# Optimization experiments

Measured on AMD Instinct MI355X. Metric: run time of the kernel, lower is better.

## Reference

```python
import jax, jax.numpy as jnp
import numpy as np

NUM_CLUSTERS = 64
NUM_ITERS = 3
TEMPERATURE = 0.1
CENTER_EMA = 0.99


def _l2norm(x, eps=1e-12):
    n = jnp.linalg.norm(x, axis=-1, keepdims=True)
    return x / jnp.maximum(n, eps)


def setup_inputs() -> dict:
    key = jax.random.key(0)
    k1, k2 = jax.random.split(key)
    B, N, d = 16, 4096, 768
    features = jax.random.normal(k1, (B, N, d), dtype=jnp.float32)
    centers = jax.random.normal(k2, (NUM_CLUSTERS, d), dtype=jnp.float32)
    return {"features": features, "centers": centers}


def reference(features, centers):
    B, N, d = features.shape
    K = centers.shape[0]
    M = B * N  # single-device: M_total == M_local

    features_norm = _l2norm(features)          # [B, N, d]
    centers_n = _l2norm(centers)               # [K, d]

    logits = jnp.einsum('bnd,kd->bnk', features_norm, centers_n) / TEMPERATURE
    Q = jnp.exp(logits.astype(jnp.float32).reshape(M, K).T)  # [K, M]

    Q = Q / jnp.maximum(Q.sum(), 1e-12)
    for _ in range(NUM_ITERS):
        row_sums = Q.sum(axis=1, keepdims=True)              # [K, 1]
        Q = Q / (jnp.maximum(row_sums, 1e-12) * float(K))
        col_sums = Q.sum(axis=0, keepdims=True)              # [1, M]
        Q = Q / (jnp.maximum(col_sums, 1e-12) * float(M))

    assignments = (Q * float(M)).T.reshape(B, N, K).astype(features.dtype)

    # EMA center update
    Q_flat = assignments.reshape(M, K)
    feat_flat = features_norm.reshape(M, d)
    weighted = jnp.einsum('mk,md->kd', Q_flat, feat_flat)    # [K, d]
    mass = Q_flat.sum(axis=0)                                # [K]
    new_centers = _l2norm(weighted / jnp.maximum(mass, 1e-6)[:, None])
    updated = CENTER_EMA * centers_n + (1.0 - CENTER_EMA) * new_centers
    updated = _l2norm(updated)

    return assignments, updated
```

## Files before the change

### kernel.cpp

```cpp
#include <hip/hip_runtime.h>
#include <hip/hip_bf16.h>

#define M_TOTAL 65536
#define DIM 768
#define KC 64
#define INV_T 10.0f

#define DT 128
#define MB 64
#define CH 8
#define MSEG 128

#define LOGITS_BLOCKS (M_TOTAL / 64)
#define SROWS 128
#define SINK_BLOCKS (M_TOTAL / SROWS)
#define PSG_ROWS 64

typedef __attribute__((ext_vector_type(4))) float f32x4;
typedef __attribute__((ext_vector_type(8))) short bf16x8;
typedef __attribute__((ext_vector_type(4))) unsigned short u16x4;

__device__ __forceinline__ short f2bf(float f) {
    __hip_bfloat16 h = __float2bfloat16(f);
    union { __hip_bfloat16 h; short s; } u; u.h = h;
    return u.s;
}

__global__ __launch_bounds__(256) void k_centers(const float* __restrict__ centers,
                                                 float* __restrict__ cn,
                                                 short* __restrict__ cnbf,
                                                 float* __restrict__ psg) {
    int k = blockIdx.x, tid = threadIdx.x;
    psg[k * 256 + tid] = 0.f;
    float ss = 0.f;
    for (int i = tid; i < DIM; i += 256) { float v = centers[k * DIM + i]; ss += v * v; }
    __shared__ float red[4];
    for (int o = 32; o; o >>= 1) ss += __shfl_xor(ss, o);
    if ((tid & 63) == 0) red[tid >> 6] = ss;
    __syncthreads();
    ss = red[0] + red[1] + red[2] + red[3];
    float inv = 1.0f / fmaxf(sqrtf(ss), 1e-12f);
    for (int i = tid; i < DIM; i += 256) {
        float v = centers[k * DIM + i] * inv;
        cn[k * DIM + i] = v;
        cnbf[k * DIM + i] = f2bf(v);
    }
}

__global__ __launch_bounds__(256) void k_logits(const float* __restrict__ F,
                                                const short* __restrict__ cnbf,
                                                float* __restrict__ E,
                                                float* __restrict__ invn,
                                                float* __restrict__ PSG0) {
    __shared__ float fbuf[3][4][1024];
    __shared__ float bsr[4][KC];
    int tid = threadIdx.x;
    int wave = tid >> 6, lane = tid & 63;
    int l15 = lane & 15, lhi = lane >> 4;
    int rowbase = blockIdx.x * 64;

    int srow_l = lane >> 4;
    int c4 = lane & 15;

#define STAGE(t_, b_)                                                                     \
    do {                                                                                  \
        _Pragma("unroll") for (int i_ = 0; i_ < 4; ++i_) {                                \
            int r_ = i_ * 4 + srow_l;                                \
            const float* src_ = F + (size_t)(rowbase + wave * 16 + r_) * DIM + (t_) * 64  \
                                + (((c4 ^ (r_ & 7)) << 2));                               \
            float* dst_ = &fbuf[b_][wave][i_ * 256];                                      \
            __builtin_amdgcn_global_load_lds(                                             \
                (const __attribute__((address_space(1))) void*)src_,                      \
                (__attribute__((address_space(3))) void*)dst_, 16, 0, 0);                 \
        }                                                                                 \
    } while (0)

    STAGE(0, 0);
    STAGE(1, 1);

    f32x4 acc[4];
#pragma unroll
    for (int n = 0; n < 4; ++n) acc[n] = (f32x4){0.f, 0.f, 0.f, 0.f};
    float ss = 0.f;

    const short* Bb = cnbf + (size_t)l15 * DIM + lhi * 8;
    int swz = (l15 & 7) << 2;

#pragma unroll
    for (int t = 0; t < 12; ++t) {
        bf16x8 b[8];
#pragma unroll
        for (int n = 0; n < 4; ++n) {
            b[n * 2]     = *(const bf16x8*)(Bb + (size_t)n * 16 * DIM + t * 64);
            b[n * 2 + 1] = *(const bf16x8*)(Bb + (size_t)n * 16 * DIM + t * 64 + 32);
        }
        if (t + 2 < 12) {
            STAGE(t + 2, (t + 2) % 3);
            asm volatile("s_waitcnt vmcnt(4)" ::: "memory");
        } else {
            asm volatile("s_waitcnt vmcnt(0)" ::: "memory");
        }
        __builtin_amdgcn_sched_barrier(0);
        const float* cb = &fbuf[t % 3][wave][l15 * 64];
#pragma unroll
        for (int kk = 0; kk < 2; ++kk) {
            int c0s = (kk * 32 + lhi * 8) ^ swz;
            f32x4 fa = *(const f32x4*)(cb + c0s);
            f32x4 fb2 = *(const f32x4*)(cb + (c0s ^ 4));
            ss += fa[0] * fa[0] + fa[1] * fa[1] + fa[2] * fa[2] + fa[3] * fa[3]
                + fb2[0] * fb2[0] + fb2[1] * fb2[1] + fb2[2] * fb2[2] + fb2[3] * fb2[3];
            bf16x8 af;
            af[0] = f2bf(fa[0]); af[1] = f2bf(fa[1]); af[2] = f2bf(fa[2]); af[3] = f2bf(fa[3]);
            af[4] = f2bf(fb2[0]); af[5] = f2bf(fb2[1]); af[6] = f2bf(fb2[2]); af[7] = f2bf(fb2[3]);
#pragma unroll
            for (int n = 0; n < 4; ++n)
                acc[n] = __builtin_amdgcn_mfma_f32_16x16x32_bf16(af, b[n * 2 + kk], acc[n], 0, 0, 0);
        }
    }
#undef STAGE

    ss += __shfl_xor(ss, 16);
    ss += __shfl_xor(ss, 32);
    float inv = 1.0f / fmaxf(sqrtf(ss), 1e-12f);
    int growbase = rowbase + wave * 16;
    if (lane < 16) invn[growbase + lane] = inv;

    float sc[4];
#pragma unroll
    for (int j = 0; j < 4; ++j) sc[j] = __shfl(inv, lhi * 4 + j) * INV_T;

    float colp[4] = {0.f, 0.f, 0.f, 0.f};
#pragma unroll
    for (int n = 0; n < 4; ++n) {
#pragma unroll
        for (int j = 0; j < 4; ++j) {
            float e = expf(acc[n][j] * sc[j]);
            int row = lhi * 4 + j;
            E[(size_t)(growbase + row) * KC + ((n * 16 + l15) ^ (row << 2))] = e;
            colp[n] += e;
        }
    }
#pragma unroll
    for (int n = 0; n < 4; ++n) {
        colp[n] += __shfl_xor(colp[n], 16);
        colp[n] += __shfl_xor(colp[n], 32);
    }
    if (lane < 16) {
#pragma unroll
        for (int n = 0; n < 4; ++n) bsr[wave][n * 16 + lane] = colp[n];
    }
    __syncthreads();
    if (tid < KC)
        atomicAdd(&PSG0[(size_t)(blockIdx.x >> 4) * KC + tid],
                  bsr[0][tid] + bsr[1][tid] + bsr[2][tid] + bsr[3][tid]);
}

template <int MODE>
__global__ __launch_bounds__(256) void k_sink(const float* __restrict__ E,
                                              const float* __restrict__ Rprev,
                                              const float* __restrict__ PSGprev,
                                              const float* __restrict__ invn,
                                              float* __restrict__ c,
                                              float* __restrict__ PSGnext,
                                              float* __restrict__ Rout,
                                              float* __restrict__ Aout,
                                              short* __restrict__ Qbf) {
    __shared__ float tile[SROWS * KC];
    __shared__ float sbuf[SROWS];
    __shared__ float Rlds[KC];
    __shared__ float bacc[4][KC];
    int tid = threadIdx.x, lane = tid & 63, wave = tid >> 6;
    int m0 = blockIdx.x * SROWS;

#pragma unroll
    for (int i = 0; i < 8; ++i) {
        const float* src = E + (size_t)(m0 + i * 16 + wave * 4 + (lane >> 4)) * KC + (lane & 15) * 4;
        float* dst = tile + (i * 16 + wave * 4) * KC;
        __builtin_amdgcn_global_load_lds((const __attribute__((address_space(1))) void*)src,
                                         (__attribute__((address_space(3))) void*)dst, 16, 0, 0);
    }

    {
        int k = tid & 63, g = tid >> 6;
        float s = 0.f;
#pragma unroll
        for (int p = 0; p < PSG_ROWS / 4; ++p) s += PSGprev[(size_t)(g + p * 4) * KC + k];
        bacc[g][k] = s;
        __syncthreads();
        if (tid < KC) {
            float sk = bacc[0][k] + bacc[1][k] + bacc[2][k] + bacc[3][k];
            float r;
            if (MODE == 0) {
                float tot = sk;
                for (int o = 32; o; o >>= 1) tot += __shfl_xor(tot, o);
                float S = fmaxf(tot, 1e-12f);
                r = (1.0f / S) / (fmaxf(sk / S, 1e-12f) * 64.0f);
            } else {
                float rp = Rprev[k];
                r = rp / (fmaxf(rp * sk, 1e-12f) * 64.0f);
            }
            Rlds[k] = r;
            if (MODE != 2) Rout[k] = r;
        }
    }
    __syncthreads();

    if (tid < SROWS) {
        const float* rp = tile + tid * KC;
        const f32x4* R4 = (const f32x4*)Rlds;
        int sw = tid & 15;
        f32x4 a = {0.f, 0.f, 0.f, 0.f};
#pragma unroll
        for (int j = 0; j < 16; ++j)
            a += *(const f32x4*)(rp + ((j ^ sw) << 2)) * R4[j];
        sbuf[tid] = a[0] + a[1] + a[2] + a[3];
    }
    __syncthreads();

    float Rl = Rlds[lane];
    float wacc = 0.f;
    int rbase = wave * 32;
#pragma unroll 4
    for (int r = 0; r < 32; ++r) {
        int rr = rbase + r;
        int m = m0 + rr;
        float e = tile[rr * KC + (lane ^ ((rr & 15) << 2))];
        float s = sbuf[rr];
        float cold = (MODE == 0) ? 1.0f : c[m];
        float cnew = cold / (fmaxf(cold * s, 1e-12f) * 65536.0f);
        if (MODE == 2) {
            float a = e * Rl * cnew * 65536.0f;
            size_t idx = (size_t)m * KC + lane;
            Aout[idx] = a;
            Qbf[idx] = f2bf(a * invn[m]);
            wacc += a;
        } else {
            if (lane == 0) c[m] = cnew;
            wacc += e * cnew;
        }
    }
    bacc[wave][lane] = wacc;
    __syncthreads();
    if (tid < KC)
        atomicAdd(&PSGnext[(size_t)(blockIdx.x >> 3) * KC + tid],
                  bacc[0][tid] + bacc[1][tid] + bacc[2][tid] + bacc[3][tid]);
}

__global__ __launch_bounds__(256) void k_weighted(const float* __restrict__ F,
                                                  const short* __restrict__ Qbf,
                                                  float* __restrict__ P) {
    __shared__ short ldsF[DT * MB];
    __shared__ short ldsQ[KC * MB];
    int tid = threadIdx.x;
    int dt = blockIdx.x;
    int ms = blockIdx.y;
    int wave = tid >> 6, lane = tid & 63;
    int l15 = lane & 15, lhi = lane >> 4;

    int m0 = ms * (MB * CH);
    int d0 = dt * DT;

    f32x4 acc[4][2];
#pragma unroll
    for (int kt = 0; kt < 4; ++kt)
#pragma unroll
        for (int ds = 0; ds < 2; ++ds) acc[kt][ds] = (f32x4){0.f, 0.f, 0.f, 0.f};

    int f_dq = (tid & 31) * 4;
    int f_m8 = (tid >> 5) * 8;
    int q_kq = (tid & 15) * 4;
    int q_m8 = ((tid >> 4) & 7) * 8;

    float4 rf[8];
    u16x4 q[8];
#define LOADCH(mb_)                                                                       \
    do {                                                                                  \
        _Pragma("unroll") for (int j = 0; j < 8; ++j)                                     \
            rf[j] = *(const float4*)(F + (size_t)((mb_) + f_m8 + j) * DIM + d0 + f_dq);   \
        if (tid < 128) {                                                                  \
            _Pragma("unroll") for (int j = 0; j < 8; ++j)                                 \
                q[j] = *(const u16x4*)(Qbf + (size_t)((mb_) + q_m8 + j) * KC + q_kq);     \
        }                                                                                 \
    } while (0)

    LOADCH(m0);
    for (int ch = 0; ch < CH; ++ch) {
        __syncthreads();
#pragma unroll
        for (int i = 0; i < 4; ++i) {
            int d = f_dq + i;
            uint4 w;
            w.x = (unsigned)(unsigned short)f2bf(rf[0][i]) | ((unsigned)(unsigned short)f2bf(rf[1][i]) << 16);
            w.y = (unsigned)(unsigned short)f2bf(rf[2][i]) | ((unsigned)(unsigned short)f2bf(rf[3][i]) << 16);
            w.z = (unsigned)(unsigned short)f2bf(rf[4][i]) | ((unsigned)(unsigned short)f2bf(rf[5][i]) << 16);
            w.w = (unsigned)(unsigned short)f2bf(rf[6][i]) | ((unsigned)(unsigned short)f2bf(rf[7][i]) << 16);
            int byte = (d * (MB * 2) + f_m8 * 2) ^ ((d & 7) << 4);
            *(uint4*)((char*)ldsF + byte) = w;
        }
        if (tid < 128) {
#pragma unroll
            for (int i = 0; i < 4; ++i) {
                int k = q_kq + i;
                uint4 w;
                w.x = (unsigned)q[0][i] | ((unsigned)q[1][i] << 16);
                w.y = (unsigned)q[2][i] | ((unsigned)q[3][i] << 16);
                w.z = (unsigned)q[4][i] | ((unsigned)q[5][i] << 16);
                w.w = (unsigned)q[6][i] | ((unsigned)q[7][i] << 16);
                int byte = (k * (MB * 2) + q_m8 * 2) ^ ((k & 7) << 4);
                *(uint4*)((char*)ldsQ + byte) = w;
            }
        }
        __syncthreads();
        if (ch + 1 < CH) LOADCH(m0 + (ch + 1) * MB);
#pragma unroll
        for (int h = 0; h < 2; ++h) {
            bf16x8 afr[4];
#pragma unroll
            for (int kt = 0; kt < 4; ++kt) {
                int k = kt * 16 + l15;
                int byte = (k * (MB * 2) + (h * 32 + lhi * 8) * 2) ^ ((k & 7) << 4);
                afr[kt] = *(bf16x8*)((char*)ldsQ + byte);
            }
#pragma unroll
            for (int ds = 0; ds < 2; ++ds) {
                int d = wave * 32 + ds * 16 + l15;
                int byte = (d * (MB * 2) + (h * 32 + lhi * 8) * 2) ^ ((d & 7) << 4);
                bf16x8 bfr = *(bf16x8*)((char*)ldsF + byte);
#pragma unroll
                for (int kt = 0; kt < 4; ++kt)
                    acc[kt][ds] = __builtin_amdgcn_mfma_f32_16x16x32_bf16(afr[kt], bfr, acc[kt][ds], 0, 0, 0);
            }
        }
    }
#undef LOADCH

    float* Pb = P + (size_t)ms * (KC * DIM) + d0;
#pragma unroll
    for (int kt = 0; kt < 4; ++kt)
#pragma unroll
        for (int ds = 0; ds < 2; ++ds) {
            int d = wave * 32 + ds * 16 + l15;
#pragma unroll
            for (int r4 = 0; r4 < 4; ++r4) {
                int k = kt * 16 + lhi * 4 + r4;
                Pb[(size_t)k * DIM + d] = acc[kt][ds][r4];
            }
        }
}

__global__ __launch_bounds__(256) void k_final(const float* __restrict__ P,
                                               const float* __restrict__ PSGM,
                                               const float* __restrict__ cn,
                                               float* __restrict__ outC) {
    int k = blockIdx.x, tid = threadIdx.x;
    __shared__ float red[4];

    float msum = (tid < PSG_ROWS) ? PSGM[(size_t)tid * KC + k] : 0.f;
    for (int o = 32; o; o >>= 1) msum += __shfl_xor(msum, o);
    if ((tid & 63) == 0) red[tid >> 6] = msum;
    __syncthreads();
    float mk = fmaxf(red[0] + red[1] + red[2] + red[3], 1e-6f);
    __syncthreads();

    float w[3];
#pragma unroll
    for (int g = 0; g < 3; ++g) {
        int d = tid + g * 256;
        const float* pp = P + (size_t)k * DIM + d;
        float s0 = 0.f, s1 = 0.f, s2 = 0.f, s3 = 0.f;
        size_t stride = (size_t)KC * DIM;
#pragma unroll 4
        for (int msg = 0; msg < MSEG; msg += 4) {
            s0 += pp[(size_t)msg * stride];
            s1 += pp[(size_t)(msg + 1) * stride];
            s2 += pp[(size_t)(msg + 2) * stride];
            s3 += pp[(size_t)(msg + 3) * stride];
        }
        w[g] = ((s0 + s1) + (s2 + s3)) / mk;
    }

    float ss = w[0] * w[0] + w[1] * w[1] + w[2] * w[2];
    for (int o = 32; o; o >>= 1) ss += __shfl_xor(ss, o);
    if ((tid & 63) == 0) red[tid >> 6] = ss;
    __syncthreads();
    ss = red[0] + red[1] + red[2] + red[3];
    float n1 = fmaxf(sqrtf(ss), 1e-12f);
    __syncthreads();

    float u0 = 0.99f * cn[k * DIM + tid]       + 0.01f * (w[0] / n1);
    float u1 = 0.99f * cn[k * DIM + tid + 256] + 0.01f * (w[1] / n1);
    float u2 = 0.99f * cn[k * DIM + tid + 512] + 0.01f * (w[2] / n1);
    float ss2 = u0 * u0 + u1 * u1 + u2 * u2;
    for (int o = 32; o; o >>= 1) ss2 += __shfl_xor(ss2, o);
    if ((tid & 63) == 0) red[tid >> 6] = ss2;
    __syncthreads();
    ss2 = red[0] + red[1] + red[2] + red[3];
    float n2 = fmaxf(sqrtf(ss2), 1e-12f);

    outC[k * DIM + tid]       = u0 / n2;
    outC[k * DIM + tid + 256] = u1 / n2;
    outC[k * DIM + tid + 512] = u2 / n2;
}

extern "C" void kernel_launch(void* const* d_in, const int* in_sizes, int n_in,
                              void* d_out, int out_size, void* d_ws, size_t ws_size,
                              hipStream_t stream) {
    const float* F = (const float*)d_in[0];
    const float* centers = (const float*)d_in[1];
    float* out = (float*)d_out;
    float* A = out;
    float* outC = out + (size_t)M_TOTAL * KC;

    float* w = (float*)d_ws;
    float* cn   = w;
    short* cnbf = (short*)(w + 49152);
    float* R0   = w + 73728;
    float* R1   = w + 73792;
    float* invn = w + 74048;
    float* cbuf = w + 139584;
    float* E    = w + 205120;
    short* Qbf  = (short*)(w + 4399424);
    float* PSG  = w + 6496576;
    float* PSG0 = PSG;
    float* PSG1 = PSG + 4096;
    float* PSG2 = PSG + 8192;
    float* PSGM = PSG + 12288;
    float* partial = w + 6520000;

    k_centers<<<KC, 256, 0, stream>>>(centers, cn, cnbf, PSG);
    k_logits<<<LOGITS_BLOCKS, 256, 0, stream>>>(F, cnbf, E, invn, PSG0);
    k_sink<0><<<SINK_BLOCKS, 256, 0, stream>>>(E, nullptr, PSG0, invn, cbuf, PSG1, R0, A, Qbf);
    k_sink<1><<<SINK_BLOCKS, 256, 0, stream>>>(E, R0, PSG1, invn, cbuf, PSG2, R1, A, Qbf);
    k_sink<2><<<SINK_BLOCKS, 256, 0, stream>>>(E, R1, PSG2, invn, cbuf, PSGM, nullptr, A, Qbf);

    dim3 wgrid(DIM / DT, MSEG);
    k_weighted<<<wgrid, 256, 0, stream>>>(F, Qbf, partial);
    k_final<<<KC, 256, 0, stream>>>(partial, PSGM, cn, outC);
}
```

Baseline: 157.2 us.

## Store bf16 Q transposed in sink kernel and read MFMA A-fragments directly from global

The final sink pass now buffers each lane's 32 bf16 Q values and writes them K-major (transposed, M contiguous) as 16-byte vectors. The weighted-sum kernel drops its Q LDS staging, transpose-packing and extra loads, and instead loads MFMA A fragments straight from the transposed global array. This removes LDS traffic and a sync-bound transpose in k_weighted. The cost is uncached, non-prefetched global loads inside the MFMA loop, which may expose latency, plus extra register pressure in k_sink.

```diff
diff --git a/kernel.cpp b/kernel.cpp
--- a/kernel.cpp
+++ b/kernel.cpp
@@ -164,7 +164,7 @@
                                               float* __restrict__ PSGnext,
                                               float* __restrict__ Rout,
                                               float* __restrict__ Aout,
-                                              short* __restrict__ Qbf) {
+                                              short* __restrict__ QbfT) {
     __shared__ float tile[SROWS * KC];
     __shared__ float sbuf[SROWS];
     __shared__ float Rlds[KC];
@@ -220,7 +220,8 @@
     float Rl = Rlds[lane];
     float wacc = 0.f;
     int rbase = wave * 32;
-#pragma unroll 4
+    short qbuf[32];
+#pragma unroll
     for (int r = 0; r < 32; ++r) {
         int rr = rbase + r;
         int m = m0 + rr;
@@ -230,15 +231,24 @@
         float cnew = cold / (fmaxf(cold * s, 1e-12f) * 65536.0f);
         if (MODE == 2) {
             float a = e * Rl * cnew * 65536.0f;
-            size_t idx = (size_t)m * KC + lane;
-            Aout[idx] = a;
-            Qbf[idx] = f2bf(a * invn[m]);
+            Aout[(size_t)m * KC + lane] = a;
+            qbuf[r] = f2bf(a * invn[m]);
             wacc += a;
         } else {
             if (lane == 0) c[m] = cnew;
             wacc += e * cnew;
         }
     }
+    if (MODE == 2) {
+        unsigned u[16];
+#pragma unroll
+        for (int i = 0; i < 16; ++i)
+            u[i] = (unsigned)(unsigned short)qbuf[2 * i] | ((unsigned)(unsigned short)qbuf[2 * i + 1] << 16);
+        uint4* dst = (uint4*)(QbfT + (size_t)lane * M_TOTAL + m0 + rbase);
+#pragma unroll
+        for (int i = 0; i < 4; ++i)
+            dst[i] = make_uint4(u[4 * i], u[4 * i + 1], u[4 * i + 2], u[4 * i + 3]);
+    }
     bacc[wave][lane] = wacc;
     __syncthreads();
     if (tid < KC)
@@ -247,10 +257,9 @@
 }
 
 __global__ __launch_bounds__(256) void k_weighted(const float* __restrict__ F,
-                                                  const short* __restrict__ Qbf,
+                                                  const short* __restrict__ QbfT,
                                                   float* __restrict__ P) {
     __shared__ short ldsF[DT * MB];
-    __shared__ short ldsQ[KC * MB];
     int tid = threadIdx.x;
     int dt = blockIdx.x;
     int ms = blockIdx.y;
@@ -268,23 +277,17 @@
 
     int f_dq = (tid & 31) * 4;
     int f_m8 = (tid >> 5) * 8;
-    int q_kq = (tid & 15) * 4;
-    int q_m8 = ((tid >> 4) & 7) * 8;
 
     float4 rf[8];
-    u16x4 q[8];
 #define LOADCH(mb_)                                                                       \
     do {                                                                                  \
         _Pragma("unroll") for (int j = 0; j < 8; ++j)                                     \
             rf[j] = *(const float4*)(F + (size_t)((mb_) + f_m8 + j) * DIM + d0 + f_dq);   \
-        if (tid < 128) {                                                                  \
-            _Pragma("unroll") for (int j = 0; j < 8; ++j)                                 \
-                q[j] = *(const u16x4*)(Qbf + (size_t)((mb_) + q_m8 + j) * KC + q_kq);     \
-        }                                                                                 \
     } while (0)
 
     LOADCH(m0);
     for (int ch = 0; ch < CH; ++ch) {
+        int mb = m0 + ch * MB;
         __syncthreads();
 #pragma unroll
         for (int i = 0; i < 4; ++i) {
@@ -297,30 +300,15 @@
             int byte = (d * (MB * 2) + f_m8 * 2) ^ ((d & 7) << 4);
             *(uint4*)((char*)ldsF + byte) = w;
         }
-        if (tid < 128) {
-#pragma unroll
-            for (int i = 0; i < 4; ++i) {
-                int k = q_kq + i;
-                uint4 w;
-                w.x = (unsigned)q[0][i] | ((unsigned)q[1][i] << 16);
-                w.y = (unsigned)q[2][i] | ((unsigned)q[3][i] << 16);
-                w.z = (unsigned)q[4][i] | ((unsigned)q[5][i] << 16);
-                w.w = (unsigned)q[6][i] | ((unsigned)q[7][i] << 16);
-                int byte = (k * (MB * 2) + q_m8 * 2) ^ ((k & 7) << 4);
-                *(uint4*)((char*)ldsQ + byte) = w;
-            }
-        }
         __syncthreads();
-        if (ch + 1 < CH) LOADCH(m0 + (ch + 1) * MB);
+        if (ch + 1 < CH) LOADCH(mb + MB);
 #pragma unroll
         for (int h = 0; h < 2; ++h) {
             bf16x8 afr[4];
 #pragma unroll
-            for (int kt = 0; kt < 4; ++kt) {
-                int k = kt * 16 + l15;
-                int byte = (k * (MB * 2) + (h * 32 + lhi * 8) * 2) ^ ((k & 7) << 4);
-                afr[kt] = *(bf16x8*)((char*)ldsQ + byte);
-            }
+            for (int kt = 0; kt < 4; ++kt)
+                afr[kt] = *(const bf16x8*)(QbfT + (size_t)(kt * 16 + l15) * M_TOTAL
+                                           + mb + h * 32 + lhi * 8);
 #pragma unroll
             for (int ds = 0; ds < 2; ++ds) {
                 int d = wave * 32 + ds * 16 + l15;
@@ -419,7 +407,7 @@
     float* invn = w + 74048;
     float* cbuf = w + 139584;
     float* E    = w + 205120;
-    short* Qbf  = (short*)(w + 4399424);
+    short* QbfT = (short*)(w + 4399424);
     float* PSG  = w + 6496576;
     float* PSG0 = PSG;
     float* PSG1 = PSG + 4096;
@@ -429,11 +417,11 @@
 
     k_centers<<<KC, 256, 0, stream>>>(centers, cn, cnbf, PSG);
     k_logits<<<LOGITS_BLOCKS, 256, 0, stream>>>(F, cnbf, E, invn, PSG0);
-    k_sink<0><<<SINK_BLOCKS, 256, 0, stream>>>(E, nullptr, PSG0, invn, cbuf, PSG1, R0, A, Qbf);
-    k_sink<1><<<SINK_BLOCKS, 256, 0, stream>>>(E, R0, PSG1, invn, cbuf, PSG2, R1, A, Qbf);
-    k_sink<2><<<SINK_BLOCKS, 256, 0, stream>>>(E, R1, PSG2, invn, cbuf, PSGM, nullptr, A, Qbf);
+    k_sink<0><<<SINK_BLOCKS, 256, 0, stream>>>(E, nullptr, PSG0, invn, cbuf, PSG1, R0, A, QbfT);
+    k_sink<1><<<SINK_BLOCKS, 256, 0, stream>>>(E, R0, PSG1, invn, cbuf, PSG2, R1, A, QbfT);
+    k_sink<2><<<SINK_BLOCKS, 256, 0, stream>>>(E, R1, PSG2, invn, cbuf, PSGM, nullptr, A, QbfT);
 
     dim3 wgrid(DIM / DT, MSEG);
-    k_weighted<<<wgrid, 256, 0, stream>>>(F, Qbf, partial);
+    k_weighted<<<wgrid, 256, 0, stream>>>(F, QbfT, partial);
     k_final<<<KC, 256, 0, stream>>>(partial, PSGM, cn, outC);
 }
```

New measurement: 162.2 us. +3.2%, slower.
